# Kernel optimization log

Measured on AMD Instinct MI355X. Metric: run time of the kernel, lower is better.

Reference implementation:

```python
import jax, jax.numpy as jnp
import numpy as np

N, FIN, H, FOUT = 4096, 128, 4, 64
NEG_INF = -1e9


def _xavier(key, shape):
    fan_in, fan_out = shape[-2], shape[-1]
    limit = float(np.sqrt(6.0 / (fan_in + fan_out)))
    return jax.random.uniform(key, shape, jnp.float32, -limit, limit)


def setup_inputs() -> dict:
    key = jax.random.key(0)
    ks = jax.random.split(key, 7)
    x = jax.random.normal(ks[0], (N, FIN), jnp.float32)
    u = jax.random.uniform(ks[1], (N, N))
    mask = jnp.where(u < 0.02, 0.0, NEG_INF).astype(jnp.float32)
    idx = jnp.arange(N)
    mask = mask.at[idx, idx].set(0.0)
    proj_param = _xavier(ks[2], (H, FIN, FOUT))          # per-head projection
    score_src = _xavier(ks[3], (H, FOUT, 1))             # scoring_fn_source (IMP1 layout)
    score_tgt = _xavier(ks[4], (H, FOUT, 1))             # scoring_fn_target
    skip_w = _xavier(ks[5], (H * FOUT, FIN))             # skip_proj Linear weight
    bias = jnp.zeros((H * FOUT,), jnp.float32)
    return {"x": x, "mask": mask, "proj_param": proj_param,
            "score_src": score_src, "score_tgt": score_tgt,
            "skip_w": skip_w, "bias": bias}


def reference(x, mask, proj_param, score_src, score_tgt, skip_w, bias):
    # project: [1,N,Fin] @ [H,Fin,Fout] -> [H,N,Fout]
    h = jnp.einsum('nf,hfo->hno', x, proj_param)
    # additive (Bahdanau-style) scores
    s_src = jnp.matmul(h, score_src)                     # [H,N,1]
    s_tgt = jnp.matmul(h, score_tgt)                     # [H,N,1]
    all_scores = jax.nn.leaky_relu(s_src + jnp.swapaxes(s_tgt, 1, 2), 0.2)  # [H,N,N]
    attn = jax.nn.softmax(all_scores + mask[None, :, :], axis=-1)           # [H,N,N]
    # aggregate: [H,N,N] @ [H,N,Fout] -> [N,H,Fout]
    out = jnp.einsum('hnm,hmo->nho', attn, h)
    # skip connection (dims differ: Fin != H*Fout -> use skip_proj)
    out = out + jnp.matmul(x, skip_w.T).reshape(N, H, FOUT)
    out = out.reshape(N, H * FOUT) + bias                # concat heads + bias
    return jax.nn.elu(out)
```

## Files before the change

kernel.cpp:

```cpp
#include <hip/hip_runtime.h>
#include <hip/hip_bf16.h>
#include <math.h>


#define NN   4096
#define FIN  128
#define NH   4
#define FO   64
#define HF   256
#define SEG  96
#define LIST 192
#define GEMM_BLOCKS 512
#define SCAN_BLOCKS 1024
#define ROWS_PER    4

typedef unsigned short ushort_t;
typedef unsigned int uint4n __attribute__((ext_vector_type(4)));

__device__ __forceinline__ ushort_t f2bf(float f) {
    __hip_bfloat16 h = __float2bfloat16(f);
    union { __hip_bfloat16 h; ushort_t u; } c; c.h = h; return c.u;
}
__device__ __forceinline__ float bf2f(ushort_t u) {
    union { unsigned int i; float f; } c; c.i = ((unsigned int)u) << 16; return c.f;
}

__global__ __launch_bounds__(256) void k0_fused(
        const float* __restrict__ x,
        const float* __restrict__ proj,
        const float* __restrict__ skw,
        const float* __restrict__ asrc,
        const float* __restrict__ atgt,
        const unsigned int* __restrict__ mask,
        ushort_t* __restrict__ h2b, float* __restrict__ skip_ws,
        float* __restrict__ src4, float* __restrict__ tgt4,
        ushort_t* __restrict__ list, int* __restrict__ cnt) {
    __shared__ float sA[64 * 68];
    __shared__ float sB[64 * 64];
    const int tid = threadIdx.x;
    const int blk = blockIdx.x;

    if (blk >= GEMM_BLOCKS) {
        ushort_t* s_nbr = (ushort_t*)sA;
        int (*s_wt)[4]  = (int(*)[4])sB;
        const int lane = tid & 63, w = tid >> 6;
        const int row0 = (blk - GEMM_BLOCKS) * ROWS_PER;
        const uint4n* mb = (const uint4n*)mask;
        const size_t wl = (size_t)(w * 256 + lane);

        uint4n cur[4], nxt[4];
        #pragma unroll
        for (int s = 0; s < 4; s++)
            cur[s] = mb[(size_t)row0 * 1024 + wl + s * 64];

        for (int rr = 0; rr < ROWS_PER; rr++) {
            const int i = row0 + rr;
            if (rr + 1 < ROWS_PER) {
                #pragma unroll
                for (int s = 0; s < 4; s++)
                    nxt[s] = mb[(size_t)(i + 1) * 1024 + wl + s * 64];
            }
            int base = 0;
            #pragma unroll
            for (int s = 0; s < 4; s++) {
                #pragma unroll
                for (int e = 0; e < 4; e++) {
                    bool hit = (cur[s][e] & 0x7fffffffu) == 0u;
                    unsigned long long bal = __ballot(hit);
                    int pre = __builtin_amdgcn_mbcnt_hi(
                                  (unsigned int)(bal >> 32),
                                  __builtin_amdgcn_mbcnt_lo((unsigned int)bal, 0));
                    if (hit) {
                        int slot = base + pre;
                        if (slot < SEG)
                            s_nbr[w * SEG + slot] =
                                (ushort_t)(w * 1024 + s * 256 + lane * 4 + e);
                    }
                    base += (int)__popcll(bal);
                }
            }
            const int p = rr & 1;
            if (lane == 0) s_wt[p][w] = base < SEG ? base : SEG;
            __syncthreads();
            const int t0 = s_wt[p][0], t1 = s_wt[p][1],
                      t2 = s_wt[p][2], t3 = s_wt[p][3];
            const int off = (w > 0 ? t0 : 0) + (w > 1 ? t1 : 0) + (w > 2 ? t2 : 0);
            const int mine = s_wt[p][w];
            ushort_t* dst = list + (size_t)i * LIST;
            for (int kk = lane; kk < mine; kk += 64) {
                int pp = off + kk;
                if (pp < LIST) dst[pp] = s_nbr[w * SEG + kk];
            }
            if (tid == 0) {
                int tot = t0 + t1 + t2 + t3;
                cnt[i] = tot < LIST ? tot : LIST;
            }
            #pragma unroll
            for (int s = 0; s < 4; s++) cur[s] = nxt[s];
        }
        return;
    }

    const int bc = blk >> 6;
    const int i0 = (blk & 63) * 64;
    const int tx = tid & 15, ty = tid >> 4;
    const int r0 = ty << 2, c0 = tx << 2;
    float acc[4][4] = {};

    #pragma unroll
    for (int kb = 0; kb < FIN; kb += 64) {
        if (kb) __syncthreads();
        #pragma unroll
        for (int q = 0; q < 4; q++) {
            int s   = tid + q * 256;
            int row = s >> 4;
            int c4  = (s & 15) << 2;
            float4 v = *(const float4*)(x + (size_t)(i0 + row) * FIN + kb + c4);
            float* d = sA + row * 68 + c4;
            d[0] = v.x; d[1] = v.y; d[2] = v.z; d[3] = v.w;
        }
        if (bc < 4) {
            const float4* src = (const float4*)(proj + (size_t)bc * FIN * FO
                                                + (size_t)kb * FO);
            #pragma unroll
            for (int q = 0; q < 4; q++) {
                int s = tid + q * 256;
                *(float4*)(sB + (size_t)s * 4) = src[s];
            }
        } else {
            const float* sw = skw + (size_t)(bc - 4) * 64 * FIN;
            #pragma unroll
            for (int q = 0; q < 4; q++) {
                int s  = tid + q * 256;
                int c  = s & 63;
                int k4 = (s >> 6) << 2;
                float4 v = *(const float4*)(sw + (size_t)c * FIN + kb + k4);
                sB[(k4 + 0) * 64 + c] = v.x;
                sB[(k4 + 1) * 64 + c] = v.y;
                sB[(k4 + 2) * 64 + c] = v.z;
                sB[(k4 + 3) * 64 + c] = v.w;
            }
        }
        __syncthreads();

        #pragma unroll 2
        for (int k = 0; k < 64; k += 4) {
            alignas(16) float a[4][4];
            alignas(16) float b[4][4];
            #pragma unroll
            for (int rr = 0; rr < 4; rr++)
                *(float4*)a[rr] = *(const float4*)(sA + (r0 + rr) * 68 + k);
            #pragma unroll
            for (int kk = 0; kk < 4; kk++)
                *(float4*)b[kk] = *(const float4*)(sB + (k + kk) * 64 + c0);
            #pragma unroll
            for (int kk = 0; kk < 4; kk++)
                #pragma unroll
                for (int rr = 0; rr < 4; rr++)
                    #pragma unroll
                    for (int cc = 0; cc < 4; cc++)
                        acc[rr][cc] = fmaf(a[rr][kk], b[kk][cc], acc[rr][cc]);
        }
    }

    if (bc < 4) {
        #pragma unroll
        for (int rr = 0; rr < 4; rr++) {
            ushort4 hv;
            hv.x = f2bf(acc[rr][0]); hv.y = f2bf(acc[rr][1]);
            hv.z = f2bf(acc[rr][2]); hv.w = f2bf(acc[rr][3]);
            *(ushort4*)(h2b + (size_t)(i0 + r0 + rr) * HF + bc * 64 + c0) = hv;
        }
        float as[4], at[4];
        #pragma unroll
        for (int cc = 0; cc < 4; cc++) {
            as[cc] = asrc[bc * FO + c0 + cc];
            at[cc] = atgt[bc * FO + c0 + cc];
        }
        #pragma unroll
        for (int rr = 0; rr < 4; rr++) {
            float ps = acc[rr][0] * as[0] + acc[rr][1] * as[1]
                     + acc[rr][2] * as[2] + acc[rr][3] * as[3];
            float pt = acc[rr][0] * at[0] + acc[rr][1] * at[1]
                     + acc[rr][2] * at[2] + acc[rr][3] * at[3];
            #pragma unroll
            for (int off = 8; off >= 1; off >>= 1) {
                ps += __shfl_xor(ps, off, 64);
                pt += __shfl_xor(pt, off, 64);
            }
            if (tx == 0) {
                int i = i0 + r0 + rr;
                src4[(size_t)i * 4 + bc] = ps;
                tgt4[(size_t)i * 4 + bc] = pt;
            }
        }
    } else {
        float* dst = skip_ws + (size_t)i0 * HF + (bc - 4) * 64;
        #pragma unroll
        for (int rr = 0; rr < 4; rr++)
            *(float4*)(dst + (size_t)(r0 + rr) * HF + c0) = *(float4*)acc[rr];
    }
}

__global__ __launch_bounds__(256) void k2b_attn(
        const ushort_t* __restrict__ list,
        const int* __restrict__ cnt,
        const ushort_t* __restrict__ h2b,
        const float* __restrict__ skip_ws,
        const float* __restrict__ src4,
        const float* __restrict__ tgt4,
        const float* __restrict__ bias,
        float* __restrict__ out) {
    __shared__ float s_p[4][LIST];
    __shared__ int   s_j[LIST];
    const int tid  = threadIdx.x;
    const int lane = tid & 63, w = tid >> 6;
    const int i    = blockIdx.x;
    const int col  = w * 64 + lane;

    const float skipv = skip_ws[(size_t)i * HF + col];
    const float bv    = bias[col];
    const float sc    = src4[(size_t)i * 4 + w];
    int c = cnt[i];
    c = c < LIST ? c : LIST;

    const ushort_t* lp = list + (size_t)i * LIST;
    for (int kk = tid; kk < c; kk += 256) s_j[kk] = lp[kk];
    __syncthreads();

    float lsum = 0.f;
    for (int kk = lane; kk < c; kk += 64) {
        int j = s_j[kk];
        float p = sc + tgt4[(size_t)j * 4 + w];
        p = p > 0.f ? p : 0.2f * p;
        p = __expf(p);
        s_p[w][kk] = p;
        lsum += p;
    }
    #pragma unroll
    for (int off = 32; off >= 1; off >>= 1)
        lsum += __shfl_xor(lsum, off, 64);
    const float inv = lsum > 0.f ? 1.0f / lsum : 0.0f;

    const ushort_t* hp = h2b + col;
    const float* ps = s_p[w];
    float acc = 0.f;
    int kk = 0;
    for (; kk + 8 <= c; kk += 8) {
        int j0 = s_j[kk + 0], j1 = s_j[kk + 1], j2 = s_j[kk + 2], j3 = s_j[kk + 3];
        int j4 = s_j[kk + 4], j5 = s_j[kk + 5], j6 = s_j[kk + 6], j7 = s_j[kk + 7];
        float p0 = ps[kk + 0], p1 = ps[kk + 1], p2 = ps[kk + 2], p3 = ps[kk + 3];
        float p4 = ps[kk + 4], p5 = ps[kk + 5], p6 = ps[kk + 6], p7 = ps[kk + 7];
        float h0 = bf2f(hp[(size_t)j0 * HF]);
        float h1 = bf2f(hp[(size_t)j1 * HF]);
        float h2v = bf2f(hp[(size_t)j2 * HF]);
        float h3 = bf2f(hp[(size_t)j3 * HF]);
        float h4 = bf2f(hp[(size_t)j4 * HF]);
        float h5 = bf2f(hp[(size_t)j5 * HF]);
        float h6 = bf2f(hp[(size_t)j6 * HF]);
        float h7 = bf2f(hp[(size_t)j7 * HF]);
        acc = fmaf(p0, h0, acc);  acc = fmaf(p1, h1, acc);
        acc = fmaf(p2, h2v, acc); acc = fmaf(p3, h3, acc);
        acc = fmaf(p4, h4, acc);  acc = fmaf(p5, h5, acc);
        acc = fmaf(p6, h6, acc);  acc = fmaf(p7, h7, acc);
    }
    for (; kk < c; kk++)
        acc = fmaf(ps[kk], bf2f(hp[(size_t)s_j[kk] * HF]), acc);

    float vv = acc * inv + skipv + bv;
    vv = vv > 0.f ? vv : expm1f(vv);
    out[(size_t)i * HF + col] = vv;
}

extern "C" void kernel_launch(void* const* d_in, const int* in_sizes, int n_in,
                              void* d_out, int out_size, void* d_ws, size_t ws_size,
                              hipStream_t stream) {
    const float*        x    = (const float*)d_in[0];
    const unsigned int* mask = (const unsigned int*)d_in[1];
    const float*        proj = (const float*)d_in[2];
    const float*        asrc = (const float*)d_in[3];
    const float*        atgt = (const float*)d_in[4];
    const float*        skw  = (const float*)d_in[5];
    const float*        bias = (const float*)d_in[6];
    float*              out  = (float*)d_out;

    char* ws = (char*)d_ws;
    ushort_t* h2b     = (ushort_t*)ws;
    float*    skip_ws = (float*)(ws + (2u << 20));
    float*    src4    = (float*)(ws + (6u << 20));
    float*    tgt4    = (float*)(ws + (6u << 20) + (64u << 10));
    ushort_t* list    = (ushort_t*)(ws + (8u << 20));
    int*      cntp    = (int*)(ws + (10u << 20));

    hipLaunchKernelGGL(k0_fused, dim3(GEMM_BLOCKS + SCAN_BLOCKS), dim3(256),
                       0, stream,
                       x, proj, skw, asrc, atgt, mask,
                       h2b, skip_ws, src4, tgt4, list, cntp);
    hipLaunchKernelGGL(k2b_attn, dim3(NN), dim3(256), 0, stream,
                       list, cntp, h2b, skip_ws, src4, tgt4, bias, out);
}
```

Measured before the change: 133.3 us.

## Store per-wave neighbor segments directly and deepen mask prefetch to two rows

```diff
diff --git a/kernel.cpp b/kernel.cpp
--- a/kernel.cpp
+++ b/kernel.cpp
@@ -9,7 +9,6 @@
 #define FO   64
 #define HF   256
 #define SEG  96
-#define LIST 192
 #define GEMM_BLOCKS 512
 #define SCAN_BLOCKS 1024
 #define ROWS_PER    4
@@ -23,6 +22,10 @@
 }
 __device__ __forceinline__ float bf2f(ushort_t u) {
     union { unsigned int i; float f; } c; c.i = ((unsigned int)u) << 16; return c.f;
+}
+__device__ __forceinline__ int mbcnt64(unsigned long long b) {
+    return __builtin_amdgcn_mbcnt_hi((unsigned int)(b >> 32),
+               __builtin_amdgcn_mbcnt_lo((unsigned int)b, 0));
 }
 
 __global__ __launch_bounds__(256) void k0_fused(
@@ -34,69 +37,54 @@
         const unsigned int* __restrict__ mask,
         ushort_t* __restrict__ h2b, float* __restrict__ skip_ws,
         float* __restrict__ src4, float* __restrict__ tgt4,
-        ushort_t* __restrict__ list, int* __restrict__ cnt) {
+        ushort_t* __restrict__ list4, int* __restrict__ cnt4) {
     __shared__ float sA[64 * 68];
     __shared__ float sB[64 * 64];
     const int tid = threadIdx.x;
     const int blk = blockIdx.x;
 
     if (blk >= GEMM_BLOCKS) {
-        ushort_t* s_nbr = (ushort_t*)sA;
-        int (*s_wt)[4]  = (int(*)[4])sB;
         const int lane = tid & 63, w = tid >> 6;
         const int row0 = (blk - GEMM_BLOCKS) * ROWS_PER;
         const uint4n* mb = (const uint4n*)mask;
         const size_t wl = (size_t)(w * 256 + lane);
 
-        uint4n cur[4], nxt[4];
+        uint4n cur[4], nx1[4], nx2[4];
         #pragma unroll
         for (int s = 0; s < 4; s++)
             cur[s] = mb[(size_t)row0 * 1024 + wl + s * 64];
+        #pragma unroll
+        for (int s = 0; s < 4; s++)
+            nx1[s] = mb[(size_t)(row0 + 1) * 1024 + wl + s * 64];
 
         for (int rr = 0; rr < ROWS_PER; rr++) {
             const int i = row0 + rr;
-            if (rr + 1 < ROWS_PER) {
+            if (rr + 2 < ROWS_PER) {
                 #pragma unroll
                 for (int s = 0; s < 4; s++)
-                    nxt[s] = mb[(size_t)(i + 1) * 1024 + wl + s * 64];
+                    nx2[s] = mb[(size_t)(i + 2) * 1024 + wl + s * 64];
             }
             int base = 0;
+            ushort_t* dst = list4 + ((size_t)i * 4 + w) * SEG;
             #pragma unroll
             for (int s = 0; s < 4; s++) {
                 #pragma unroll
                 for (int e = 0; e < 4; e++) {
                     bool hit = (cur[s][e] & 0x7fffffffu) == 0u;
                     unsigned long long bal = __ballot(hit);
-                    int pre = __builtin_amdgcn_mbcnt_hi(
-                                  (unsigned int)(bal >> 32),
-                                  __builtin_amdgcn_mbcnt_lo((unsigned int)bal, 0));
+                    int pre = mbcnt64(bal);
                     if (hit) {
                         int slot = base + pre;
                         if (slot < SEG)
-                            s_nbr[w * SEG + slot] =
+                            dst[slot] =
                                 (ushort_t)(w * 1024 + s * 256 + lane * 4 + e);
                     }
                     base += (int)__popcll(bal);
                 }
             }
-            const int p = rr & 1;
-            if (lane == 0) s_wt[p][w] = base < SEG ? base : SEG;
-            __syncthreads();
-            const int t0 = s_wt[p][0], t1 = s_wt[p][1],
-                      t2 = s_wt[p][2], t3 = s_wt[p][3];
-            const int off = (w > 0 ? t0 : 0) + (w > 1 ? t1 : 0) + (w > 2 ? t2 : 0);
-            const int mine = s_wt[p][w];
-            ushort_t* dst = list + (size_t)i * LIST;
-            for (int kk = lane; kk < mine; kk += 64) {
-                int pp = off + kk;
-                if (pp < LIST) dst[pp] = s_nbr[w * SEG + kk];
-            }
-            if (tid == 0) {
-                int tot = t0 + t1 + t2 + t3;
-                cnt[i] = tot < LIST ? tot : LIST;
-            }
-            #pragma unroll
-            for (int s = 0; s < 4; s++) cur[s] = nxt[s];
+            if (lane == 0) cnt4[i * 4 + w] = base < SEG ? base : SEG;
+            #pragma unroll
+            for (int s = 0; s < 4; s++) { cur[s] = nx1[s]; nx1[s] = nx2[s]; }
         }
         return;
     }
@@ -203,16 +191,16 @@
 }
 
 __global__ __launch_bounds__(256) void k2b_attn(
-        const ushort_t* __restrict__ list,
-        const int* __restrict__ cnt,
+        const ushort_t* __restrict__ list4,
+        const int* __restrict__ cnt4,
         const ushort_t* __restrict__ h2b,
         const float* __restrict__ skip_ws,
         const float* __restrict__ src4,
         const float* __restrict__ tgt4,
         const float* __restrict__ bias,
         float* __restrict__ out) {
-    __shared__ float s_p[4][LIST];
-    __shared__ int   s_j[LIST];
+    __shared__ float s_p[4][4 * SEG];
+    __shared__ int   s_j[4 * SEG];
     const int tid  = threadIdx.x;
     const int lane = tid & 63, w = tid >> 6;
     const int i    = blockIdx.x;
@@ -221,21 +209,31 @@
     const float skipv = skip_ws[(size_t)i * HF + col];
     const float bv    = bias[col];
     const float sc    = src4[(size_t)i * 4 + w];
-    int c = cnt[i];
-    c = c < LIST ? c : LIST;
-
-    const ushort_t* lp = list + (size_t)i * LIST;
-    for (int kk = tid; kk < c; kk += 256) s_j[kk] = lp[kk];
+    int cts[4];
+    #pragma unroll
+    for (int s = 0; s < 4; s++) {
+        int c = cnt4[i * 4 + s];
+        cts[s] = c < SEG ? c : SEG;
+    }
+
+    {
+        const ushort_t* lp = list4 + ((size_t)i * 4 + w) * SEG;
+        for (int kk = lane; kk < cts[w]; kk += 64)
+            s_j[w * SEG + kk] = lp[kk];
+    }
     __syncthreads();
 
     float lsum = 0.f;
-    for (int kk = lane; kk < c; kk += 64) {
-        int j = s_j[kk];
-        float p = sc + tgt4[(size_t)j * 4 + w];
-        p = p > 0.f ? p : 0.2f * p;
-        p = __expf(p);
-        s_p[w][kk] = p;
-        lsum += p;
+    #pragma unroll
+    for (int s = 0; s < 4; s++) {
+        for (int kk = lane; kk < cts[s]; kk += 64) {
+            int j = s_j[s * SEG + kk];
+            float p = sc + tgt4[(size_t)j * 4 + w];
+            p = p > 0.f ? p : 0.2f * p;
+            p = __expf(p);
+            s_p[w][s * SEG + kk] = p;
+            lsum += p;
+        }
     }
     #pragma unroll
     for (int off = 32; off >= 1; off >>= 1)
@@ -243,29 +241,34 @@
     const float inv = lsum > 0.f ? 1.0f / lsum : 0.0f;
 
     const ushort_t* hp = h2b + col;
-    const float* ps = s_p[w];
     float acc = 0.f;
-    int kk = 0;
-    for (; kk + 8 <= c; kk += 8) {
-        int j0 = s_j[kk + 0], j1 = s_j[kk + 1], j2 = s_j[kk + 2], j3 = s_j[kk + 3];
-        int j4 = s_j[kk + 4], j5 = s_j[kk + 5], j6 = s_j[kk + 6], j7 = s_j[kk + 7];
-        float p0 = ps[kk + 0], p1 = ps[kk + 1], p2 = ps[kk + 2], p3 = ps[kk + 3];
-        float p4 = ps[kk + 4], p5 = ps[kk + 5], p6 = ps[kk + 6], p7 = ps[kk + 7];
-        float h0 = bf2f(hp[(size_t)j0 * HF]);
-        float h1 = bf2f(hp[(size_t)j1 * HF]);
-        float h2v = bf2f(hp[(size_t)j2 * HF]);
-        float h3 = bf2f(hp[(size_t)j3 * HF]);
-        float h4 = bf2f(hp[(size_t)j4 * HF]);
-        float h5 = bf2f(hp[(size_t)j5 * HF]);
-        float h6 = bf2f(hp[(size_t)j6 * HF]);
-        float h7 = bf2f(hp[(size_t)j7 * HF]);
-        acc = fmaf(p0, h0, acc);  acc = fmaf(p1, h1, acc);
-        acc = fmaf(p2, h2v, acc); acc = fmaf(p3, h3, acc);
-        acc = fmaf(p4, h4, acc);  acc = fmaf(p5, h5, acc);
-        acc = fmaf(p6, h6, acc);  acc = fmaf(p7, h7, acc);
-    }
-    for (; kk < c; kk++)
-        acc = fmaf(ps[kk], bf2f(hp[(size_t)s_j[kk] * HF]), acc);
+    #pragma unroll
+    for (int s = 0; s < 4; s++) {
+        const int ct = cts[s];
+        const int* nb = s_j + s * SEG;
+        const float* ps = s_p[w] + s * SEG;
+        int kk = 0;
+        for (; kk + 8 <= ct; kk += 8) {
+            int j0 = nb[kk + 0], j1 = nb[kk + 1], j2 = nb[kk + 2], j3 = nb[kk + 3];
+            int j4 = nb[kk + 4], j5 = nb[kk + 5], j6 = nb[kk + 6], j7 = nb[kk + 7];
+            float p0 = ps[kk + 0], p1 = ps[kk + 1], p2 = ps[kk + 2], p3 = ps[kk + 3];
+            float p4 = ps[kk + 4], p5 = ps[kk + 5], p6 = ps[kk + 6], p7 = ps[kk + 7];
+            float h0 = bf2f(hp[(size_t)j0 * HF]);
+            float h1 = bf2f(hp[(size_t)j1 * HF]);
+            float h2v = bf2f(hp[(size_t)j2 * HF]);
+            float h3 = bf2f(hp[(size_t)j3 * HF]);
+            float h4 = bf2f(hp[(size_t)j4 * HF]);
+            float h5 = bf2f(hp[(size_t)j5 * HF]);
+            float h6 = bf2f(hp[(size_t)j6 * HF]);
+            float h7 = bf2f(hp[(size_t)j7 * HF]);
+            acc = fmaf(p0, h0, acc);  acc = fmaf(p1, h1, acc);
+            acc = fmaf(p2, h2v, acc); acc = fmaf(p3, h3, acc);
+            acc = fmaf(p4, h4, acc);  acc = fmaf(p5, h5, acc);
+            acc = fmaf(p6, h6, acc);  acc = fmaf(p7, h7, acc);
+        }
+        for (; kk < ct; kk++)
+            acc = fmaf(ps[kk], bf2f(hp[(size_t)nb[kk] * HF]), acc);
+    }
 
     float vv = acc * inv + skipv + bv;
     vv = vv > 0.f ? vv : expm1f(vv);
@@ -289,13 +292,13 @@
     float*    skip_ws = (float*)(ws + (2u << 20));
     float*    src4    = (float*)(ws + (6u << 20));
     float*    tgt4    = (float*)(ws + (6u << 20) + (64u << 10));
-    ushort_t* list    = (ushort_t*)(ws + (8u << 20));
-    int*      cntp    = (int*)(ws + (10u << 20));
+    ushort_t* list4   = (ushort_t*)(ws + (8u << 20));
+    int*      cnt4p   = (int*)(ws + (11u << 20) + (512u << 10));
 
     hipLaunchKernelGGL(k0_fused, dim3(GEMM_BLOCKS + SCAN_BLOCKS), dim3(256),
                        0, stream,
                        x, proj, skw, asrc, atgt, mask,
-                       h2b, skip_ws, src4, tgt4, list, cntp);
+                       h2b, skip_ws, src4, tgt4, list4, cnt4p);
     hipLaunchKernelGGL(k2b_attn, dim3(NN), dim3(256), 0, stream,
-                       list, cntp, h2b, skip_ws, src4, tgt4, bias, out);
-}
+                       list4, cnt4p, h2b, skip_ws, src4, tgt4, bias, out);
+}
```

After: 140.3 us. +5.3%, slower.
